# Kernel optimization log

Hardware: AMD Instinct MI355X
Metric: run time of the kernel (lower is better)

## Reference

```python
import jax, jax.numpy as jnp
import numpy as np
from jax import lax

DIM = 512          # model dim
L = 32             # img_size
N = L * L          # tokens
H = 4              # heads
C = DIM // 4       # channels per Res2Net scale
D = C // H         # per-head dim = 32 (== dim_head)
B = 8
SCALE = 32 ** -0.5  # dim_head ** -0.5
EPS = 1e-5


def setup_inputs() -> dict:
    key = jax.random.key(0)
    ks = jax.random.split(key, 13)
    nrm = lambda k, s, std: jax.random.normal(k, s, jnp.float32) * std
    uni = lambda k, s: jax.random.uniform(k, s, jnp.float32, 0.5, 1.5)
    return {
        "x": nrm(ks[0], (B, N, DIM), 1.0),
        "w_in": nrm(ks[1], (DIM, DIM), DIM ** -0.5),
        "bn1_g": uni(ks[2], (DIM,)),
        "bn1_b": nrm(ks[3], (DIM,), 0.1),
        "bn1_m": nrm(ks[4], (DIM,), 0.1),
        "bn1_v": uni(ks[5], (DIM,)),
        "w_dw": nrm(ks[6], (C, 1, 3, 3), 1.0 / 3.0),
        "w_pw": nrm(ks[7], (C, C), C ** -0.5),
        "bn2_g": uni(ks[8], (C,)),
        "bn2_b": nrm(ks[9], (C,), 0.1),
        "bn2_m": nrm(ks[10], (C,), 0.1),
        "bn2_v": uni(ks[11], (C,)),
        "w_out": nrm(ks[12], (DIM, DIM), DIM ** -0.5),
    }


def _bn(x, g, b, m, v):
    # eval-mode BatchNorm2d over NCHW
    inv = g / jnp.sqrt(v + EPS)
    return x * inv[None, :, None, None] + (b - m * inv)[None, :, None, None]


def _forward(x, w_in, bn1_g, bn1_b, bn1_m, bn1_v,
             w_dw, w_pw, bn2_g, bn2_b, bn2_m, bn2_v, w_out):
    b = x.shape[0]
    # 'b (l w) n -> b n l w'
    xi = x.transpose(0, 2, 1).reshape(b, DIM, L, L)
    # Res2Net: inconv (1x1 conv + BN)
    ident = jnp.einsum('oc,bchw->bohw', w_in, xi)
    ident = _bn(ident, bn1_g, bn1_b, bn1_m, bn1_v)
    xs = jnp.split(ident, 4, axis=1)

    def x3conv(t):
        t = lax.conv_general_dilated(
            t, w_dw, window_strides=(1, 1), padding='SAME',
            feature_group_count=C,
            dimension_numbers=('NCHW', 'OIHW', 'NCHW'))
        t = jnp.einsum('oc,bchw->bohw', w_pw, t)
        return _bn(t, bn2_g, bn2_b, bn2_m, bn2_v)

    ys = [xs[0]]
    ys.append(x3conv(xs[1]))
    ys.append(x3conv(xs[2] + ys[1]))
    ys.append(x3conv(xs[3] + ys[2]))
    y = jnp.stack(ys, axis=1)  # [b, 4, C, L, L]

    # 'b (h d) l w -> b h (l w) d' per scale; batch the 4 scales together
    qkv = y.reshape(b, 4, H, D, N).transpose(0, 1, 2, 4, 3)  # [b,4,h,n,d]
    att = jnp.einsum('bshid,bshjd->bshij', qkv, qkv) * SCALE   # [b,4,h,n,n]
    att = jax.nn.softmax(att, axis=-1)
    o = jnp.einsum('bshij,bshjd->bshid', att, qkv)             # [b,4,h,n,d]
    # cat over scales of 'b h n d -> b n (h d)' => [b, n, (s h d)] = [b, n, DIM]
    o = o.transpose(0, 3, 1, 2, 4).reshape(b, N, DIM)
    return o @ w_out.T  # Linear(dim, dim, bias=False); dropout is identity (eval)


def reference(x, w_in, bn1_g, bn1_b, bn1_m, bn1_v,
              w_dw, w_pw, bn2_g, bn2_b, bn2_m, bn2_v, w_out):
    return _forward(x, w_in, bn1_g, bn1_b, bn1_m, bn1_v,
                    w_dw, w_pw, bn2_g, bn2_b, bn2_m, bn2_v, w_out)
```

## Files before the change

### kernel.cpp

```cpp
#include <hip/hip_runtime.h>
#include <hip/hip_bf16.h>


#define DIMM 512
#define NTOK 1024
#define CC   128
#define DD   32
#define BB   8
#define EPSB 1e-5f
#define SCALE_ATT 0.17677669529663687f
#define K2EXP (SCALE_ATT * 1.4426950408889634f)
#define TJ 128

typedef __attribute__((ext_vector_type(8))) short short8;
typedef __attribute__((ext_vector_type(4))) float f32x4;

__device__ __forceinline__ unsigned short f2bf(float f) {
    unsigned int x = __float_as_uint(f);
    unsigned int r = x + 0x7fffu + ((x >> 16) & 1u);
    return (unsigned short)(r >> 16);
}
__device__ __forceinline__ unsigned int f2bf2(float lo, float hi) {
    return (unsigned int)f2bf(lo) | ((unsigned int)f2bf(hi) << 16);
}

__global__ __launch_bounds__(256) void k_mm_in(
    const float* __restrict__ w_in,
    const float* __restrict__ x,
    const float* __restrict__ g1, const float* __restrict__ b1,
    const float* __restrict__ m1, const float* __restrict__ v1,
    float* __restrict__ Y)
{
    __shared__ __align__(16) unsigned short As[128][72];
    __shared__ __align__(16) unsigned short Bs[128][72];
    const int r0 = blockIdx.x * 128;
    const int o0 = blockIdx.y * 128;
    const int b  = r0 >> 10, nloc0 = r0 & 1023;
    const int t = threadIdx.x, wid = t >> 6, lane = t & 63;
    const int l16 = lane & 15, quad = lane >> 4;
    const int wm = (wid >> 1) * 64, wn = (wid & 1) * 64;

    f32x4 acc[4][4];
#pragma unroll
    for (int i = 0; i < 4; i++)
#pragma unroll
        for (int j = 0; j < 4; j++) acc[i][j] = (f32x4){0.f, 0.f, 0.f, 0.f};

    for (int k0 = 0; k0 < DIMM; k0 += 64) {
        __syncthreads();
#pragma unroll
        for (int it = 0; it < 8; it++) {
            int flat = it * 256 + t;
            int row = flat >> 4, c4 = flat & 15;
            float4 w4 = *(const float4*)&w_in[(size_t)(o0 + row) * DIMM + k0 + c4 * 4];
            *(uint2*)&As[row][c4 * 4] = make_uint2(f2bf2(w4.x, w4.y), f2bf2(w4.z, w4.w));
            float4 x4 = *(const float4*)&x[(size_t)(r0 + row) * DIMM + k0 + c4 * 4];
            *(uint2*)&Bs[row][c4 * 4] = make_uint2(f2bf2(x4.x, x4.y), f2bf2(x4.z, x4.w));
        }
        __syncthreads();
#pragma unroll
        for (int kk = 0; kk < 2; kk++) {
            short8 af[4], bf_[4];
#pragma unroll
            for (int i = 0; i < 4; i++) af[i]  = *(const short8*)&As[wm + i * 16 + l16][kk * 32 + quad * 8];
#pragma unroll
            for (int j = 0; j < 4; j++) bf_[j] = *(const short8*)&Bs[wn + j * 16 + l16][kk * 32 + quad * 8];
#pragma unroll
            for (int i = 0; i < 4; i++)
#pragma unroll
                for (int j = 0; j < 4; j++)
                    acc[i][j] = __builtin_amdgcn_mfma_f32_16x16x32_bf16(af[i], bf_[j], acc[i][j], 0, 0, 0);
        }
    }
#pragma unroll
    for (int i = 0; i < 4; i++)
#pragma unroll
        for (int r = 0; r < 4; r++) {
            int o = o0 + wm + i * 16 + quad * 4 + r;
            float inv  = g1[o] / sqrtf(v1[o] + EPSB);
            float beta = b1[o] - m1[o] * inv;
#pragma unroll
            for (int j = 0; j < 4; j++) {
                int n = nloc0 + wn + j * 16 + l16;
                Y[((size_t)b * DIMM + o) * NTOK + n] = acc[i][j][r] * inv + beta;
            }
        }
}

__global__ __launch_bounds__(256) void k_dwconv(
    const float* __restrict__ Y, const float* __restrict__ w_dw,
    float* __restrict__ tmp, int s)
{
    __shared__ float img[34][34];
    const int c = blockIdx.x;
    const int b = blockIdx.y;
    const int t = threadIdx.x;
    for (int i = t; i < 34 * 34; i += 256) (&img[0][0])[i] = 0.f;
    __syncthreads();
    const float* src0 = Y + ((size_t)b * DIMM + s * CC + c) * NTOK;
    const float* src1 = (s >= 2) ? (Y + ((size_t)b * DIMM + (s - 1) * CC + c) * NTOK) : nullptr;
    for (int p = t; p < NTOK; p += 256) {
        float v = src0[p];
        if (src1) v += src1[p];
        img[(p >> 5) + 1][(p & 31) + 1] = v;
    }
    __syncthreads();
    float w[9];
#pragma unroll
    for (int i = 0; i < 9; i++) w[i] = w_dw[c * 9 + i];
    for (int p = t; p < NTOK; p += 256) {
        int yy = p >> 5, xx = p & 31;
        float s0 = 0.f;
#pragma unroll
        for (int ky = 0; ky < 3; ky++)
#pragma unroll
            for (int kx = 0; kx < 3; kx++)
                s0 += img[yy + ky][xx + kx] * w[ky * 3 + kx];
        tmp[((size_t)b * CC + c) * NTOK + p] = s0;
    }
}

__global__ __launch_bounds__(256) void k_mm_pw(
    const float* __restrict__ tmp, const float* __restrict__ w_pw,
    const float* __restrict__ g2, const float* __restrict__ b2,
    const float* __restrict__ m2, const float* __restrict__ v2,
    float* __restrict__ Y, int s)
{
    __shared__ __align__(16) unsigned short As[128][72];
    __shared__ __align__(16) unsigned short Bs[64][72];
    const int n0 = blockIdx.x * 64;
    const int b  = blockIdx.y;
    const int t = threadIdx.x, wid = t >> 6, lane = t & 63;
    const int l16 = lane & 15, quad = lane >> 4;
    const int wm = (wid >> 1) * 64, wn = (wid & 1) * 32;

    f32x4 acc[4][2];
#pragma unroll
    for (int i = 0; i < 4; i++) { acc[i][0] = (f32x4){0.f,0.f,0.f,0.f}; acc[i][1] = (f32x4){0.f,0.f,0.f,0.f}; }

    for (int k0 = 0; k0 < CC; k0 += 64) {
        __syncthreads();
#pragma unroll
        for (int it = 0; it < 8; it++) {
            int flat = it * 256 + t;
            int row = flat >> 4, c4 = flat & 15;
            float4 w4 = *(const float4*)&w_pw[(size_t)row * CC + k0 + c4 * 4];
            *(uint2*)&As[row][c4 * 4] = make_uint2(f2bf2(w4.x, w4.y), f2bf2(w4.z, w4.w));
        }
#pragma unroll
        for (int it = 0; it < 4; it++) {
            int flat = it * 256 + t;
            int c = flat >> 4, n4 = (flat & 15) * 4;
            float4 v = *(const float4*)&tmp[((size_t)b * CC + k0 + c) * NTOK + n0 + n4];
            Bs[n4 + 0][c] = f2bf(v.x);
            Bs[n4 + 1][c] = f2bf(v.y);
            Bs[n4 + 2][c] = f2bf(v.z);
            Bs[n4 + 3][c] = f2bf(v.w);
        }
        __syncthreads();
#pragma unroll
        for (int kk = 0; kk < 2; kk++) {
            short8 af[4], bf_[2];
#pragma unroll
            for (int i = 0; i < 4; i++) af[i]  = *(const short8*)&As[wm + i * 16 + l16][kk * 32 + quad * 8];
#pragma unroll
            for (int j = 0; j < 2; j++) bf_[j] = *(const short8*)&Bs[wn + j * 16 + l16][kk * 32 + quad * 8];
#pragma unroll
            for (int i = 0; i < 4; i++)
#pragma unroll
                for (int j = 0; j < 2; j++)
                    acc[i][j] = __builtin_amdgcn_mfma_f32_16x16x32_bf16(af[i], bf_[j], acc[i][j], 0, 0, 0);
        }
    }
#pragma unroll
    for (int i = 0; i < 4; i++)
#pragma unroll
        for (int r = 0; r < 4; r++) {
            int o = wm + i * 16 + quad * 4 + r;
            float inv  = g2[o] / sqrtf(v2[o] + EPSB);
            float beta = b2[o] - m2[o] * inv;
#pragma unroll
            for (int j = 0; j < 2; j++) {
                int n = n0 + wn + j * 16 + l16;
                Y[((size_t)b * DIMM + s * CC + o) * NTOK + n] = acc[i][j][r] * inv + beta;
            }
        }
}

__global__ __launch_bounds__(256) void k_prep(
    const float* __restrict__ Y,
    unsigned short* __restrict__ Vp,
    unsigned short* __restrict__ Qt)
{
    __shared__ float T[32][129];
    const int jt = blockIdx.x;
    const int n0 = jt * 128;
    const int g  = blockIdx.y;
    const int b = g >> 4, s = (g >> 2) & 3, h = g & 3;
    const int cb = s * CC + h * DD;
    const int t = threadIdx.x;
#pragma unroll
    for (int k = 0; k < 8; k++) {
        int idx = k * 256 + t;
        int d = idx >> 6, jp = (idx & 63) * 2;
        float2 v = *(const float2*)&Y[((size_t)b * DIMM + cb + d) * NTOK + n0 + jp];
        T[d][jp] = v.x; T[d][jp + 1] = v.y;
    }
    __syncthreads();
#pragma unroll
    for (int k = 0; k < 8; k++) {
        int idx = k * 256 + t;
        int n = idx >> 4, dp = (idx & 15) * 2;
        *(unsigned int*)&Qt[((size_t)g * NTOK + n0 + n) * DD + dp] = f2bf2(T[dp][n], T[dp + 1][n]);
    }
#pragma unroll
    for (int e2 = 0; e2 < 2; e2++) {
        int e = e2 * 256 + t;
        int sub = e >> 6, lane = e & 63;
        int quad = lane >> 4, l16 = lane & 15;
        int d  = (sub & 1) * 16 + l16;
        int jb = (sub >> 1) * 32 + quad * 4;
        uint4 v;
        v.x = f2bf2(T[d][jb + 0],  T[d][jb + 1]);
        v.y = f2bf2(T[d][jb + 2],  T[d][jb + 3]);
        v.z = f2bf2(T[d][jb + 16], T[d][jb + 17]);
        v.w = f2bf2(T[d][jb + 18], T[d][jb + 19]);
        *(uint4*)&Vp[((((size_t)g * 8 + jt) * 8 + sub) * 64 + lane) * 8] = v;
    }
}

__global__ __launch_bounds__(256) void k_attn(
    const unsigned short* __restrict__ Qtg,
    const unsigned short* __restrict__ Vp,
    unsigned short* __restrict__ Ob)
{
    const int blk = blockIdx.x;
    const int g = blk & 127, ib = blk >> 7;
    const int b = g >> 4;
    const int s = (g >> 2) & 3, h = g & 3;
    const int cb = s * CC + h * DD;
    const unsigned short* Qt = Qtg + (size_t)g * NTOK * DD;
    const unsigned short* Vg = Vp + (size_t)g * 8 * 8 * 64 * 8;
    const int t = threadIdx.x;
    const int wid = t >> 6, lane = t & 63;
    const int l16 = lane & 15, quad = lane >> 4;
    const int i0 = ib * 128 + wid * 16 + l16;
    const int i1 = i0 + 64;

    const short8 qi0 = *(const short8*)&Qt[(size_t)i0 * DD + quad * 8];
    const short8 qi1 = *(const short8*)&Qt[(size_t)i1 * DD + quad * 8];
    const short8 ones = {0x3F80, 0x3F80, 0x3F80, 0x3F80, 0x3F80, 0x3F80, 0x3F80, 0x3F80};

    float dq0 = 0.f, dq1 = 0.f;
#pragma unroll
    for (int e = 0; e < 8; e++) {
        float v0 = __uint_as_float(((unsigned int)(unsigned short)qi0[e]) << 16);
        float v1 = __uint_as_float(((unsigned int)(unsigned short)qi1[e]) << 16);
        dq0 = fmaf(v0, v0, dq0);
        dq1 = fmaf(v1, v1, dq1);
    }
    dq0 += __shfl_xor(dq0, 16); dq0 += __shfl_xor(dq0, 32);
    dq1 += __shfl_xor(dq1, 16); dq1 += __shfl_xor(dq1, 32);
    const float mnk0 = dq0 * K2EXP;
    const float mnk1 = dq1 * K2EXP;

    f32x4 lacc0 = {0.f,0.f,0.f,0.f}, lacc1 = {0.f,0.f,0.f,0.f};
    f32x4 oacc0[2] = {{0.f,0.f,0.f,0.f},{0.f,0.f,0.f,0.f}};
    f32x4 oacc1[2] = {{0.f,0.f,0.f,0.f},{0.f,0.f,0.f,0.f}};
    const f32x4 zero4 = {0.f, 0.f, 0.f, 0.f};

#pragma unroll 2
    for (int jt = 0; jt < 8; jt++) {
        const int j0 = jt * TJ;
        short8 pb0[4], pb1[4];
#pragma unroll
        for (int jb = 0; jb < 8; jb++) {
            short8 qj = *(const short8*)&Qt[(size_t)(j0 + jb * 16 + l16) * DD + quad * 8];
            f32x4 s0 = __builtin_amdgcn_mfma_f32_16x16x32_bf16(qj, qi0, zero4, 0, 0, 0);
            f32x4 s1 = __builtin_amdgcn_mfma_f32_16x16x32_bf16(qj, qi1, zero4, 0, 0, 0);
            float a0 = __builtin_amdgcn_exp2f(fmaf(s0[0], K2EXP, -mnk0));
            float a1 = __builtin_amdgcn_exp2f(fmaf(s0[1], K2EXP, -mnk0));
            float a2 = __builtin_amdgcn_exp2f(fmaf(s0[2], K2EXP, -mnk0));
            float a3 = __builtin_amdgcn_exp2f(fmaf(s0[3], K2EXP, -mnk0));
            ((unsigned int*)&pb0[jb >> 1])[(jb & 1) * 2] =
                __builtin_amdgcn_perm(__float_as_uint(a1), __float_as_uint(a0), 0x07060302u);
            ((unsigned int*)&pb0[jb >> 1])[(jb & 1) * 2 + 1] =
                __builtin_amdgcn_perm(__float_as_uint(a3), __float_as_uint(a2), 0x07060302u);
            float c0 = __builtin_amdgcn_exp2f(fmaf(s1[0], K2EXP, -mnk1));
            float c1 = __builtin_amdgcn_exp2f(fmaf(s1[1], K2EXP, -mnk1));
            float c2 = __builtin_amdgcn_exp2f(fmaf(s1[2], K2EXP, -mnk1));
            float c3 = __builtin_amdgcn_exp2f(fmaf(s1[3], K2EXP, -mnk1));
            ((unsigned int*)&pb1[jb >> 1])[(jb & 1) * 2] =
                __builtin_amdgcn_perm(__float_as_uint(c1), __float_as_uint(c0), 0x07060302u);
            ((unsigned int*)&pb1[jb >> 1])[(jb & 1) * 2 + 1] =
                __builtin_amdgcn_perm(__float_as_uint(c3), __float_as_uint(c2), 0x07060302u);
        }

#pragma unroll
        for (int wp = 0; wp < 4; wp++) {
            short8 af0 = *(const short8*)&Vg[(((size_t)jt * 8 + wp * 2 + 0) * 64 + lane) * 8];
            short8 af1 = *(const short8*)&Vg[(((size_t)jt * 8 + wp * 2 + 1) * 64 + lane) * 8];
            oacc0[0] = __builtin_amdgcn_mfma_f32_16x16x32_bf16(af0, pb0[wp], oacc0[0], 0, 0, 0);
            oacc0[1] = __builtin_amdgcn_mfma_f32_16x16x32_bf16(af1, pb0[wp], oacc0[1], 0, 0, 0);
            lacc0    = __builtin_amdgcn_mfma_f32_16x16x32_bf16(ones, pb0[wp], lacc0, 0, 0, 0);
            oacc1[0] = __builtin_amdgcn_mfma_f32_16x16x32_bf16(af0, pb1[wp], oacc1[0], 0, 0, 0);
            oacc1[1] = __builtin_amdgcn_mfma_f32_16x16x32_bf16(af1, pb1[wp], oacc1[1], 0, 0, 0);
            lacc1    = __builtin_amdgcn_mfma_f32_16x16x32_bf16(ones, pb1[wp], lacc1, 0, 0, 0);
        }
    }

    float invl0 = 1.f / lacc0[0];
    float invl1 = 1.f / lacc1[0];
#pragma unroll
    for (int dblk = 0; dblk < 2; dblk++) {
        uint2 pkd;
        pkd.x = f2bf2(oacc0[dblk][0] * invl0, oacc0[dblk][1] * invl0);
        pkd.y = f2bf2(oacc0[dblk][2] * invl0, oacc0[dblk][3] * invl0);
        *(uint2*)&Ob[((size_t)b * NTOK + i0) * DIMM + cb + dblk * 16 + quad * 4] = pkd;
        pkd.x = f2bf2(oacc1[dblk][0] * invl1, oacc1[dblk][1] * invl1);
        pkd.y = f2bf2(oacc1[dblk][2] * invl1, oacc1[dblk][3] * invl1);
        *(uint2*)&Ob[((size_t)b * NTOK + i1) * DIMM + cb + dblk * 16 + quad * 4] = pkd;
    }
}

__global__ __launch_bounds__(256) void k_mm_out(
    const unsigned short* __restrict__ Oin,
    const float* __restrict__ w_out,
    float* __restrict__ out)
{
    __shared__ __align__(16) unsigned short As[128][72];
    __shared__ __align__(16) unsigned short Bs[128][72];
    const int r0 = blockIdx.x * 128;
    const int o0 = blockIdx.y * 128;
    const int t = threadIdx.x, wid = t >> 6, lane = t & 63;
    const int l16 = lane & 15, quad = lane >> 4;
    const int wm = (wid >> 1) * 64, wn = (wid & 1) * 64;

    f32x4 acc[4][4];
#pragma unroll
    for (int i = 0; i < 4; i++)
#pragma unroll
        for (int j = 0; j < 4; j++) acc[i][j] = (f32x4){0.f, 0.f, 0.f, 0.f};

    for (int k0 = 0; k0 < DIMM; k0 += 64) {
        __syncthreads();
#pragma unroll
        for (int q = 0; q < 4; q++) {
            int flat = q * 256 + t;
            int row = flat >> 3, c8 = flat & 7;
            *(short8*)&As[row][c8 * 8] = *(const short8*)&Oin[(size_t)(r0 + row) * DIMM + k0 + c8 * 8];
        }
#pragma unroll
        for (int it = 0; it < 8; it++) {
            int flat = it * 256 + t;
            int row = flat >> 4, c4 = flat & 15;
            float4 w4 = *(const float4*)&w_out[(size_t)(o0 + row) * DIMM + k0 + c4 * 4];
            *(uint2*)&Bs[row][c4 * 4] = make_uint2(f2bf2(w4.x, w4.y), f2bf2(w4.z, w4.w));
        }
        __syncthreads();
#pragma unroll
        for (int kk = 0; kk < 2; kk++) {
            short8 af[4], bf_[4];
#pragma unroll
            for (int i = 0; i < 4; i++) af[i]  = *(const short8*)&As[wm + i * 16 + l16][kk * 32 + quad * 8];
#pragma unroll
            for (int j = 0; j < 4; j++) bf_[j] = *(const short8*)&Bs[wn + j * 16 + l16][kk * 32 + quad * 8];
#pragma unroll
            for (int i = 0; i < 4; i++)
#pragma unroll
                for (int j = 0; j < 4; j++)
                    acc[i][j] = __builtin_amdgcn_mfma_f32_16x16x32_bf16(af[i], bf_[j], acc[i][j], 0, 0, 0);
        }
    }
#pragma unroll
    for (int i = 0; i < 4; i++)
#pragma unroll
        for (int r = 0; r < 4; r++) {
            int rr = r0 + wm + i * 16 + quad * 4 + r;
#pragma unroll
            for (int j = 0; j < 4; j++) {
                int o = o0 + wn + j * 16 + l16;
                out[(size_t)rr * DIMM + o] = acc[i][j][r];
            }
        }
}

extern "C" void kernel_launch(void* const* d_in, const int* in_sizes, int n_in,
                              void* d_out, int out_size, void* d_ws, size_t ws_size,
                              hipStream_t stream)
{
    const float* x    = (const float*)d_in[0];
    const float* w_in = (const float*)d_in[1];
    const float* g1   = (const float*)d_in[2];
    const float* b1   = (const float*)d_in[3];
    const float* m1   = (const float*)d_in[4];
    const float* v1   = (const float*)d_in[5];
    const float* wdw  = (const float*)d_in[6];
    const float* wpw  = (const float*)d_in[7];
    const float* g2   = (const float*)d_in[8];
    const float* b2   = (const float*)d_in[9];
    const float* m2   = (const float*)d_in[10];
    const float* v2   = (const float*)d_in[11];
    const float* wout = (const float*)d_in[12];
    float* out = (float*)d_out;

    char* base = (char*)d_ws;
    float*          Y   = (float*)base;
    unsigned short* Ob  = (unsigned short*)base;
    float*          tmp = (float*)(base + (size_t)16 * 1024 * 1024);
    unsigned short* Vp  = (unsigned short*)(base + (size_t)16 * 1024 * 1024);
    unsigned short* Qt  = (unsigned short*)(base + (size_t)24 * 1024 * 1024);

    k_mm_in<<<dim3(64, 4), 256, 0, stream>>>(w_in, x, g1, b1, m1, v1, Y);
    for (int s = 1; s <= 3; s++) {
        k_dwconv<<<dim3(CC, BB), 256, 0, stream>>>(Y, wdw, tmp, s);
        k_mm_pw<<<dim3(16, 8), 256, 0, stream>>>(tmp, wpw, g2, b2, m2, v2, Y, s);
    }
    k_prep<<<dim3(8, 128), 256, 0, stream>>>(Y, Vp, Qt);
    k_attn<<<dim3(1024), 256, 0, stream>>>(Qt, Vp, Ob);
    k_mm_out<<<dim3(64, 4), 256, 0, stream>>>(Ob, wout, out);
}
```

Measured before the change: 197.1 us.

## Fuse depthwise 3x3 conv into pointwise matmul kernel per scale

Replaces the separate depthwise-conv and pointwise-matmul kernels with one kernel. Each block loads a 64-token tile plus a one-row halo on each side for all 128 channels, computes the 3x3 conv in shared memory as bf16, and writes the result straight into the MFMA B-operand tile. This removes the fp32 tmp round trip through global memory and one launch per scale. In exchange the conv input is rounded to bf16 before the stencil, and each block reads halo rows that neighbouring blocks also read.

```diff
diff --git a/kernel.cpp b/kernel.cpp
--- a/kernel.cpp
+++ b/kernel.cpp
@@ -23,6 +23,9 @@
 __device__ __forceinline__ unsigned int f2bf2(float lo, float hi) {
     return (unsigned int)f2bf(lo) | ((unsigned int)f2bf(hi) << 16);
 }
+__device__ __forceinline__ float bf2f(unsigned short u) {
+    return __uint_as_float(((unsigned int)u) << 16);
+}
 
 __global__ __launch_bounds__(256) void k_mm_in(
     const float* __restrict__ w_in,
@@ -87,53 +90,78 @@
         }
 }
 
-__global__ __launch_bounds__(256) void k_dwconv(
-    const float* __restrict__ Y, const float* __restrict__ w_dw,
-    float* __restrict__ tmp, int s)
-{
-    __shared__ float img[34][34];
-    const int c = blockIdx.x;
-    const int b = blockIdx.y;
-    const int t = threadIdx.x;
-    for (int i = t; i < 34 * 34; i += 256) (&img[0][0])[i] = 0.f;
-    __syncthreads();
-    const float* src0 = Y + ((size_t)b * DIMM + s * CC + c) * NTOK;
-    const float* src1 = (s >= 2) ? (Y + ((size_t)b * DIMM + (s - 1) * CC + c) * NTOK) : nullptr;
-    for (int p = t; p < NTOK; p += 256) {
-        float v = src0[p];
-        if (src1) v += src1[p];
-        img[(p >> 5) + 1][(p & 31) + 1] = v;
-    }
-    __syncthreads();
-    float w[9];
-#pragma unroll
-    for (int i = 0; i < 9; i++) w[i] = w_dw[c * 9 + i];
-    for (int p = t; p < NTOK; p += 256) {
-        int yy = p >> 5, xx = p & 31;
-        float s0 = 0.f;
-#pragma unroll
-        for (int ky = 0; ky < 3; ky++)
-#pragma unroll
-            for (int kx = 0; kx < 3; kx++)
-                s0 += img[yy + ky][xx + kx] * w[ky * 3 + kx];
-        tmp[((size_t)b * CC + c) * NTOK + p] = s0;
-    }
-}
-
-__global__ __launch_bounds__(256) void k_mm_pw(
-    const float* __restrict__ tmp, const float* __restrict__ w_pw,
+#define FU_OFF_BS  32768
+#define FU_OFF_WDW (32768 + 2 * 64 * 72 * 2)
+#define FU_SMEM    (FU_OFF_WDW + 128 * 9 * 4)
+
+__global__ __launch_bounds__(256) void k_fused(
+    const float* __restrict__ Y_in,
+    const float* __restrict__ w_dw,
+    const float* __restrict__ w_pw,
     const float* __restrict__ g2, const float* __restrict__ b2,
     const float* __restrict__ m2, const float* __restrict__ v2,
     float* __restrict__ Y, int s)
 {
-    __shared__ __align__(16) unsigned short As[128][72];
-    __shared__ __align__(16) unsigned short Bs[64][72];
-    const int n0 = blockIdx.x * 64;
+    __shared__ __align__(16) unsigned char SM[FU_SMEM];
+    unsigned short (*Fin)[4][32] = (unsigned short (*)[4][32])SM;
+    unsigned short (*As)[72]     = (unsigned short (*)[72])SM;
+    unsigned short (*Bs)[64][72] = (unsigned short (*)[64][72])(SM + FU_OFF_BS);
+    float* Wdw = (float*)(SM + FU_OFF_WDW);
+
+    const int bx = blockIdx.x;
+    const int n0 = bx * 64;
     const int b  = blockIdx.y;
     const int t = threadIdx.x, wid = t >> 6, lane = t & 63;
     const int l16 = lane & 15, quad = lane >> 4;
+
+#pragma unroll
+    for (int it = 0; it < 5; it++) {
+        int idx = it * 256 + t;
+        if (idx < 128 * 9) Wdw[idx] = w_dw[idx];
+    }
+    const float* src0 = Y_in + ((size_t)b * DIMM + s * CC) * NTOK;
+    const float* src1 = Y_in + ((size_t)b * DIMM + (s - 1) * CC) * NTOK;
+#pragma unroll
+    for (int it = 0; it < 16; it++) {
+        int flat = it * 256 + t;
+        int c = flat >> 5, q = flat & 31;
+        int n_in = n0 - 32 + q * 4;
+        float4 v = make_float4(0.f, 0.f, 0.f, 0.f);
+        if ((unsigned)n_in < (unsigned)NTOK) {
+            v = *(const float4*)&src0[(size_t)c * NTOK + n_in];
+            if (s >= 2) {
+                float4 u = *(const float4*)&src1[(size_t)c * NTOK + n_in];
+                v.x += u.x; v.y += u.y; v.z += u.z; v.w += u.w;
+            }
+        }
+        *(uint2*)&Fin[c][q >> 3][(q & 7) * 4] = make_uint2(f2bf2(v.x, v.y), f2bf2(v.z, v.w));
+    }
+    __syncthreads();
+
+    {
+        const int lr = lane >> 5, col = lane & 31;
+#pragma unroll 4
+        for (int cc = 0; cc < 32; cc++) {
+            int c = wid * 32 + cc;
+            const float* w = &Wdw[c * 9];
+            float s0 = 0.f;
+#pragma unroll
+            for (int ky = 0; ky < 3; ky++) {
+                int fr = lr + ky;
+                float vm = 0.f, vp = 0.f;
+                if (col > 0)  vm = bf2f(Fin[c][fr][col - 1]);
+                float v0 = bf2f(Fin[c][fr][col]);
+                if (col < 31) vp = bf2f(Fin[c][fr][col + 1]);
+                s0 = fmaf(vm, w[ky * 3 + 0], s0);
+                s0 = fmaf(v0, w[ky * 3 + 1], s0);
+                s0 = fmaf(vp, w[ky * 3 + 2], s0);
+            }
+            Bs[c >> 6][lr * 32 + col][c & 63] = f2bf(s0);
+        }
+    }
+    __syncthreads();
+
     const int wm = (wid >> 1) * 64, wn = (wid & 1) * 32;
-
     f32x4 acc[4][2];
 #pragma unroll
     for (int i = 0; i < 4; i++) { acc[i][0] = (f32x4){0.f,0.f,0.f,0.f}; acc[i][1] = (f32x4){0.f,0.f,0.f,0.f}; }
@@ -147,24 +175,15 @@
             float4 w4 = *(const float4*)&w_pw[(size_t)row * CC + k0 + c4 * 4];
             *(uint2*)&As[row][c4 * 4] = make_uint2(f2bf2(w4.x, w4.y), f2bf2(w4.z, w4.w));
         }
-#pragma unroll
-        for (int it = 0; it < 4; it++) {
-            int flat = it * 256 + t;
-            int c = flat >> 4, n4 = (flat & 15) * 4;
-            float4 v = *(const float4*)&tmp[((size_t)b * CC + k0 + c) * NTOK + n0 + n4];
-            Bs[n4 + 0][c] = f2bf(v.x);
-            Bs[n4 + 1][c] = f2bf(v.y);
-            Bs[n4 + 2][c] = f2bf(v.z);
-            Bs[n4 + 3][c] = f2bf(v.w);
-        }
-        __syncthreads();
+        __syncthreads();
+        const int half = k0 >> 6;
 #pragma unroll
         for (int kk = 0; kk < 2; kk++) {
             short8 af[4], bf_[2];
 #pragma unroll
             for (int i = 0; i < 4; i++) af[i]  = *(const short8*)&As[wm + i * 16 + l16][kk * 32 + quad * 8];
 #pragma unroll
-            for (int j = 0; j < 2; j++) bf_[j] = *(const short8*)&Bs[wn + j * 16 + l16][kk * 32 + quad * 8];
+            for (int j = 0; j < 2; j++) bf_[j] = *(const short8*)&Bs[half][wn + j * 16 + l16][kk * 32 + quad * 8];
 #pragma unroll
             for (int i = 0; i < 4; i++)
 #pragma unroll
@@ -407,14 +426,12 @@
     char* base = (char*)d_ws;
     float*          Y   = (float*)base;
     unsigned short* Ob  = (unsigned short*)base;
-    float*          tmp = (float*)(base + (size_t)16 * 1024 * 1024);
     unsigned short* Vp  = (unsigned short*)(base + (size_t)16 * 1024 * 1024);
     unsigned short* Qt  = (unsigned short*)(base + (size_t)24 * 1024 * 1024);
 
     k_mm_in<<<dim3(64, 4), 256, 0, stream>>>(w_in, x, g1, b1, m1, v1, Y);
     for (int s = 1; s <= 3; s++) {
-        k_dwconv<<<dim3(CC, BB), 256, 0, stream>>>(Y, wdw, tmp, s);
-        k_mm_pw<<<dim3(16, 8), 256, 0, stream>>>(tmp, wpw, g2, b2, m2, v2, Y, s);
+        k_fused<<<dim3(16, 8), 256, 0, stream>>>(Y, wdw, wpw, g2, b2, m2, v2, Y, s);
     }
     k_prep<<<dim3(8, 128), 256, 0, stream>>>(Y, Vp, Qt);
     k_attn<<<dim3(1024), 256, 0, stream>>>(Qt, Vp, Ob);
```

Measured after the change: 232.6 us. 18.1% more time.

## Double-buffer K and V tiles in LDS via async global-to-LDS loads

Applied to the files above, without the earlier changes.

The attention kernel now stages each 128-key tile of K and V into double-buffered shared memory with direct global-to-LDS loads, prefetching the next tile while the current one is processed. K rows use an XOR swizzle to avoid bank conflicts. Previously every wave read K and V straight from global memory, so the four waves each fetched the same data redundantly. The change adds a block-wide barrier per tile and drops the unroll-2 pragma, which may reduce instruction-level overlap.

```diff
diff --git a/kernel.cpp b/kernel.cpp
--- a/kernel.cpp
+++ b/kernel.cpp
@@ -22,6 +22,11 @@
 }
 __device__ __forceinline__ unsigned int f2bf2(float lo, float hi) {
     return (unsigned int)f2bf(lo) | ((unsigned int)f2bf(hi) << 16);
+}
+__device__ __forceinline__ void gl_lds16(const void* g, void* l) {
+    __builtin_amdgcn_global_load_lds(
+        (const __attribute__((address_space(1))) unsigned int*)g,
+        (__attribute__((address_space(3))) unsigned int*)l, 16, 0, 0);
 }
 
 __global__ __launch_bounds__(256) void k_mm_in(
@@ -234,6 +239,9 @@
     const unsigned short* __restrict__ Vp,
     unsigned short* __restrict__ Ob)
 {
+    __shared__ __align__(16) unsigned short Kt[2][128][32];
+    __shared__ __align__(16) unsigned short Vt[2][8][64][8];
+
     const int blk = blockIdx.x;
     const int g = blk & 127, ib = blk >> 7;
     const int b = g >> 4;
@@ -251,6 +259,10 @@
     const short8 qi1 = *(const short8*)&Qt[(size_t)i1 * DD + quad * 8];
     const short8 ones = {0x3F80, 0x3F80, 0x3F80, 0x3F80, 0x3F80, 0x3F80, 0x3F80, 0x3F80};
 
+    const int krow_l = lane >> 2;
+    const int kgcol  = ((lane & 3) ^ ((lane >> 3) & 3)) * 8;
+    const int kswz = (quad ^ ((l16 >> 1) & 3)) * 8;
+
     float dq0 = 0.f, dq1 = 0.f;
 #pragma unroll
     for (int e = 0; e < 8; e++) {
@@ -269,13 +281,30 @@
     f32x4 oacc1[2] = {{0.f,0.f,0.f,0.f},{0.f,0.f,0.f,0.f}};
     const f32x4 zero4 = {0.f, 0.f, 0.f, 0.f};
 
-#pragma unroll 2
+    auto stage = [&](int bsel, int jt_) {
+#pragma unroll
+        for (int c = 0; c < 2; c++) {
+            int grow = jt_ * TJ + wid * 32 + c * 16 + krow_l;
+            gl_lds16(&Qt[(size_t)grow * DD + kgcol], &Kt[bsel][wid * 32 + c * 16][0]);
+        }
+#pragma unroll
+        for (int c = 0; c < 2; c++) {
+            int sub = wid * 2 + c;
+            gl_lds16(&Vg[(((size_t)jt_ * 8 + sub) * 64 + lane) * 8], &Vt[bsel][sub][0][0]);
+        }
+    };
+
+    stage(0, 0);
+    __syncthreads();
+
     for (int jt = 0; jt < 8; jt++) {
-        const int j0 = jt * TJ;
+        const int cur = jt & 1;
+        if (jt < 7) stage(cur ^ 1, jt + 1);
+
         short8 pb0[4], pb1[4];
 #pragma unroll
         for (int jb = 0; jb < 8; jb++) {
-            short8 qj = *(const short8*)&Qt[(size_t)(j0 + jb * 16 + l16) * DD + quad * 8];
+            short8 qj = *(const short8*)&Kt[cur][jb * 16 + l16][kswz];
             f32x4 s0 = __builtin_amdgcn_mfma_f32_16x16x32_bf16(qj, qi0, zero4, 0, 0, 0);
             f32x4 s1 = __builtin_amdgcn_mfma_f32_16x16x32_bf16(qj, qi1, zero4, 0, 0, 0);
             float a0 = __builtin_amdgcn_exp2f(fmaf(s0[0], K2EXP, -mnk0));
@@ -298,8 +327,8 @@
 
 #pragma unroll
         for (int wp = 0; wp < 4; wp++) {
-            short8 af0 = *(const short8*)&Vg[(((size_t)jt * 8 + wp * 2 + 0) * 64 + lane) * 8];
-            short8 af1 = *(const short8*)&Vg[(((size_t)jt * 8 + wp * 2 + 1) * 64 + lane) * 8];
+            short8 af0 = *(const short8*)&Vt[cur][wp * 2 + 0][lane][0];
+            short8 af1 = *(const short8*)&Vt[cur][wp * 2 + 1][lane][0];
             oacc0[0] = __builtin_amdgcn_mfma_f32_16x16x32_bf16(af0, pb0[wp], oacc0[0], 0, 0, 0);
             oacc0[1] = __builtin_amdgcn_mfma_f32_16x16x32_bf16(af1, pb0[wp], oacc0[1], 0, 0, 0);
             lacc0    = __builtin_amdgcn_mfma_f32_16x16x32_bf16(ones, pb0[wp], lacc0, 0, 0, 0);
@@ -307,6 +336,8 @@
             oacc1[1] = __builtin_amdgcn_mfma_f32_16x16x32_bf16(af1, pb1[wp], oacc1[1], 0, 0, 0);
             lacc1    = __builtin_amdgcn_mfma_f32_16x16x32_bf16(ones, pb1[wp], lacc1, 0, 0, 0);
         }
+
+        __syncthreads();
     }
 
     float invl0 = 1.f / lacc0[0];
```

New measurement: 194.2 us. No clear change (-1.4%).
